# Kernel optimization log

Measured on AMD Instinct MI355X. Metric: run time of the kernel, lower is better.

Reference implementation:

```python
import jax, jax.numpy as jnp
import numpy as np

K_HOPS = 2  # number_layers


def _gcn_norm(edge_index, edge_weight, num_nodes):
    # add self loops with weight 1 (PyG gcn_norm default, fill_value=1)
    row, col = edge_index[0], edge_index[1]
    loop = jnp.arange(num_nodes, dtype=edge_index.dtype)
    row = jnp.concatenate([row, loop])
    col = jnp.concatenate([col, loop])
    w = jnp.concatenate([edge_weight, jnp.ones((num_nodes,), edge_weight.dtype)])
    deg = jax.ops.segment_sum(w, col, num_segments=num_nodes)
    dinv = jnp.where(deg > 0, jax.lax.rsqrt(deg), 0.0)
    norm = dinv[row] * w * dinv[col]
    return row, col, norm


def setup_inputs() -> dict:
    key = jax.random.key(0)
    k1, k2, k3, k4 = jax.random.split(key, 4)
    N, E, F_IN, F_OUT = 100000, 1600000, 256, 40
    x = jax.random.normal(k1, (N, F_IN), dtype=jnp.float32)
    edge_index = jax.random.randint(k2, (2, E), 0, N, dtype=jnp.int64)
    edge_attr = jax.random.uniform(k3, (E,), dtype=jnp.float32)
    W = jax.random.normal(k4, (F_OUT, F_IN), dtype=jnp.float32) * (1.0 / np.sqrt(F_IN))
    b = jnp.zeros((F_OUT,), dtype=jnp.float32)
    return {"x": x, "edge_index": edge_index, "edge_attr": edge_attr, "W": W, "b": b}


def reference(x, edge_index, edge_attr, W, b):
    N = x.shape[0]
    row, col, norm = _gcn_norm(edge_index, edge_attr, N)
    for _ in range(K_HOPS):
        x = jax.ops.segment_sum(norm[:, None] * x[row], col, num_segments=N)
    out = x @ W.T + b           # SGConv final linear
    out = jax.nn.relu(out)      # dropout is a no-op in eval mode
    return jax.nn.log_softmax(out, axis=-1)
```

## Files before the change

kernel.cpp:

```cpp
#include <hip/hip_runtime.h>
#include <hip/hip_bf16.h>
#include <math.h>

#define TF_IN   256
#define TF_OUT  40
#define NCHUNK  (TF_OUT / 4)
#define BCAP    48
#define WQ      32767.0f


__device__ inline float bf2f(unsigned short u) {
    union { unsigned int i; float f; } t; t.i = ((unsigned int)u) << 16; return t.f;
}
__device__ inline unsigned short f2bf(float f) {
    union { float f; unsigned int i; } t; t.f = f;
    unsigned int r = t.i + 0x7FFF + ((t.i >> 16) & 1);
    return (unsigned short)(r >> 16);
}

__global__ void zero_kernel(int* __restrict__ cnt, int N) {
    int i = blockIdx.x * blockDim.x + threadIdx.x;
    if (i < N) cnt[i] = 0;
}

__global__ __launch_bounds__(256) void fused_gemm_scatter_kernel(
        const float* __restrict__ x, const float* __restrict__ W,
        unsigned short* __restrict__ h, int N, int gemmBlocks,
        const int* __restrict__ row, const int* __restrict__ col,
        const float* __restrict__ w, int* __restrict__ cnt,
        unsigned int* __restrict__ bucket, int E) {
    __shared__ float4 xs[128][8];
    __shared__ float4 wsm[40][9];
    int tid = threadIdx.x;

    if ((int)blockIdx.x < gemmBlocks) {
        int ng = tid >> 2;
        int jg = tid & 3;
        int j0 = jg * 10;
        int nodeBase = blockIdx.x * 128;
        int sk = (ng >> 1) & 7;

        float acc[2][10];
#pragma unroll
        for (int i = 0; i < 2; ++i)
#pragma unroll
            for (int j = 0; j < 10; ++j) acc[i][j] = 0.f;

        const float4* x4 = (const float4*)x;
        const float4* W4 = (const float4*)W;

        for (int kt = 0; kt < 8; ++kt) {
            int kb4 = kt * 8;
#pragma unroll
            for (int i = 0; i < 4; ++i) {
                int idx = tid + i * 256;
                int n = idx >> 3, c4 = idx & 7;
                int gn = nodeBase + n;
                float4 v = make_float4(0.f, 0.f, 0.f, 0.f);
                if (gn < N) v = x4[(size_t)gn * (TF_IN / 4) + kb4 + c4];
                xs[n][c4 ^ ((n >> 2) & 7)] = v;
            }
            {
                int idx = tid;
                int j = idx >> 3, c4 = idx & 7;
                wsm[j][c4] = W4[(size_t)j * (TF_IN / 4) + kb4 + c4];
                if (tid < 64) {
                    idx = tid + 256;
                    j = idx >> 3; c4 = idx & 7;
                    wsm[j][c4] = W4[(size_t)j * (TF_IN / 4) + kb4 + c4];
                }
            }
            __syncthreads();
#pragma unroll 2
            for (int c4 = 0; c4 < 8; ++c4) {
                int phys = c4 ^ sk;
                float4 xv0 = xs[ng * 2][phys];
                float4 xv1 = xs[ng * 2 + 1][phys];
#pragma unroll
                for (int jj = 0; jj < 10; ++jj) {
                    float4 wv = wsm[j0 + jj][c4];
                    acc[0][jj] += xv0.x * wv.x + xv0.y * wv.y + xv0.z * wv.z + xv0.w * wv.w;
                    acc[1][jj] += xv1.x * wv.x + xv1.y * wv.y + xv1.z * wv.z + xv1.w * wv.w;
                }
            }
            __syncthreads();
        }

#pragma unroll
        for (int i = 0; i < 2; ++i) {
            int gn = nodeBase + ng * 2 + i;
            if (gn < N) {
                ushort2* hp2 = (ushort2*)(h + (size_t)gn * TF_OUT + j0);
#pragma unroll
                for (int p = 0; p < 5; ++p) {
                    ushort2 o;
                    o.x = f2bf(acc[i][2 * p]);
                    o.y = f2bf(acc[i][2 * p + 1]);
                    hp2[p] = o;
                }
            }
        }
    } else {
        int e = (blockIdx.x - gemmBlocks) * 256 + tid;
        if (e < E) {
            int c = col[e];
            int pos = atomicAdd(&cnt[c], 1);
            if (pos < BCAP) {
                unsigned int wq = (unsigned int)(w[e] * WQ + 0.5f);
                bucket[(size_t)c * BCAP + pos] = ((unsigned int)row[e] << 15) | wq;
            }
        }
    }
}

__global__ void deg_kernel(const unsigned int* __restrict__ bucket, const int* __restrict__ cnt,
                           float* __restrict__ dinv, int N) {
    int n = blockIdx.x * blockDim.x + threadIdx.x;
    if (n >= N) return;
    int m = cnt[n]; if (m > BCAP) m = BCAP;
    const unsigned int* b = bucket + (size_t)n * BCAP;
    float s = 1.0f;
    for (int k = 0; k < m; ++k) s += (float)(b[k] & 0x7FFF) * (1.0f / WQ);
    dinv[n] = rsqrtf(s);
}

__global__ void hop_bf_kernel(const ushort4* __restrict__ hin, ushort4* __restrict__ hout,
                              const int* __restrict__ cnt, const unsigned int* __restrict__ bucket,
                              const float* __restrict__ dinv, int N) {
    int t = blockIdx.x * blockDim.x + threadIdx.x;
    int node  = t / NCHUNK;
    int chunk = t % NCHUNK;
    if (node >= N) return;

    float d = dinv[node];
    ushort4 a = hin[(size_t)node * NCHUNK + chunk];
    float4 acc = make_float4(bf2f(a.x) * d, bf2f(a.y) * d, bf2f(a.z) * d, bf2f(a.w) * d);

    int m = cnt[node]; if (m > BCAP) m = BCAP;
    const unsigned int* b = bucket + (size_t)node * BCAP;
    for (int k = 0; k < m; ++k) {
        unsigned int e = b[k];
        unsigned int r = e >> 15;
        float v = dinv[r] * ((float)(e & 0x7FFF) * (1.0f / WQ));
        ushort4 hv = hin[(size_t)r * NCHUNK + chunk];
        acc.x += v * bf2f(hv.x);
        acc.y += v * bf2f(hv.y);
        acc.z += v * bf2f(hv.z);
        acc.w += v * bf2f(hv.w);
    }
    ushort4 o;
    o.x = f2bf(acc.x * d); o.y = f2bf(acc.y * d);
    o.z = f2bf(acc.z * d); o.w = f2bf(acc.w * d);
    hout[(size_t)node * NCHUNK + chunk] = o;
}

__global__ void hop_f32_kernel(const ushort4* __restrict__ hin, float4* __restrict__ hout,
                               const int* __restrict__ cnt, const unsigned int* __restrict__ bucket,
                               const float* __restrict__ dinv, int N) {
    int t = blockIdx.x * blockDim.x + threadIdx.x;
    int node  = t / NCHUNK;
    int chunk = t % NCHUNK;
    if (node >= N) return;

    float d = dinv[node];
    ushort4 a = hin[(size_t)node * NCHUNK + chunk];
    float4 acc = make_float4(bf2f(a.x) * d, bf2f(a.y) * d, bf2f(a.z) * d, bf2f(a.w) * d);

    int m = cnt[node]; if (m > BCAP) m = BCAP;
    const unsigned int* b = bucket + (size_t)node * BCAP;
    for (int k = 0; k < m; ++k) {
        unsigned int e = b[k];
        unsigned int r = e >> 15;
        float v = dinv[r] * ((float)(e & 0x7FFF) * (1.0f / WQ));
        ushort4 hv = hin[(size_t)r * NCHUNK + chunk];
        acc.x += v * bf2f(hv.x);
        acc.y += v * bf2f(hv.y);
        acc.z += v * bf2f(hv.z);
        acc.w += v * bf2f(hv.w);
    }
    float4 o = make_float4(acc.x * d, acc.y * d, acc.z * d, acc.w * d);
    hout[(size_t)node * NCHUNK + chunk] = o;
}

__global__ void epilogue_kernel(float* __restrict__ out, const float* __restrict__ b, int N) {
    int n = blockIdx.x * blockDim.x + threadIdx.x;
    if (n >= N) return;
    float4* o4 = (float4*)out + (size_t)n * NCHUNK;
    float v[TF_OUT];
#pragma unroll
    for (int i = 0; i < NCHUNK; ++i) {
        float4 t = o4[i];
        v[4 * i] = t.x; v[4 * i + 1] = t.y; v[4 * i + 2] = t.z; v[4 * i + 3] = t.w;
    }
    float m = -1e30f;
#pragma unroll
    for (int j = 0; j < TF_OUT; ++j) {
        float t = v[j] + b[j];
        t = fmaxf(t, 0.f);
        v[j] = t;
        m = fmaxf(m, t);
    }
    float s = 0.f;
#pragma unroll
    for (int j = 0; j < TF_OUT; ++j) s += __expf(v[j] - m);
    float lse = m + __logf(s);
#pragma unroll
    for (int i = 0; i < NCHUNK; ++i) {
        float4 t;
        t.x = v[4 * i]     - lse;
        t.y = v[4 * i + 1] - lse;
        t.z = v[4 * i + 2] - lse;
        t.w = v[4 * i + 3] - lse;
        o4[i] = t;
    }
}

extern "C" void kernel_launch(void* const* d_in, const int* in_sizes, int n_in,
                              void* d_out, int out_size, void* d_ws, size_t ws_size,
                              hipStream_t stream) {
    const float* x  = (const float*)d_in[0];
    const int*   ei = (const int*)d_in[1];
    const float* ew = (const float*)d_in[2];
    const float* W  = (const float*)d_in[3];
    const float* b  = (const float*)d_in[4];

    const int F_out = in_sizes[4];
    const int F_in  = in_sizes[3] / F_out;
    const int N     = in_sizes[0] / F_in;
    const int E     = in_sizes[2];
    const int* row = ei;
    const int* col = ei + E;

    char* ws = (char*)d_ws;
    size_t off = 0;
    auto alloc = [&](size_t bytes) {
        void* p = ws + off;
        off += (bytes + 255) & ~(size_t)255;
        return p;
    };

    int*          cnt    = (int*)          alloc((size_t)N * 4);
    float*        dinv   = (float*)        alloc((size_t)N * 4);
    unsigned int* bucket = (unsigned int*) alloc((size_t)N * BCAP * 4);
    unsigned short* h0   = (unsigned short*)alloc((size_t)N * TF_OUT * 2);
    unsigned short* h1   = (unsigned short*)alloc((size_t)N * TF_OUT * 2);

    const int tb = 256;
    hipLaunchKernelGGL(zero_kernel, dim3((N + tb - 1) / tb), dim3(tb), 0, stream, cnt, N);

    int gemmBlocks    = (N + 127) / 128;
    int scatterBlocks = (E + 255) / 256;
    hipLaunchKernelGGL(fused_gemm_scatter_kernel, dim3(gemmBlocks + scatterBlocks), dim3(256),
                       0, stream, x, W, h0, N, gemmBlocks, row, col, ew, cnt, bucket, E);

    hipLaunchKernelGGL(deg_kernel, dim3((N + tb - 1) / tb), dim3(tb), 0, stream,
                       bucket, cnt, dinv, N);
    int hopThreads = N * NCHUNK;
    hipLaunchKernelGGL(hop_bf_kernel, dim3((hopThreads + tb - 1) / tb), dim3(tb), 0, stream,
                       (const ushort4*)h0, (ushort4*)h1, cnt, bucket, dinv, N);
    hipLaunchKernelGGL(hop_f32_kernel, dim3((hopThreads + tb - 1) / tb), dim3(tb), 0, stream,
                       (const ushort4*)h1, (float4*)d_out, cnt, bucket, dinv, N);
    hipLaunchKernelGGL(epilogue_kernel, dim3((N + tb - 1) / tb), dim3(tb), 0, stream,
                       (float*)d_out, b, N);
}
```

Measured before the change: 352.3 us.

## Fuse second hop with log-softmax epilogue and widen gather to 8-wide chunks

Each thread in the hop kernels now gathers 8 bf16 features (16-byte loads) instead of 4, and the bucket loop is unrolled by 4 with vector index loads to expose more memory-level parallelism. The second hop is fused with bias, ReLU and log-softmax using a shared-memory reduction across the 5 threads per node, which removes the fp32 intermediate write and reread. The edge scatter now handles 4 edges per thread with vectorized loads. The trade-offs are more registers per thread and fewer threads in flight for the gather.

```diff
diff --git a/kernel.cpp b/kernel.cpp
--- a/kernel.cpp
+++ b/kernel.cpp
@@ -4,10 +4,12 @@
 
 #define TF_IN   256
 #define TF_OUT  40
-#define NCHUNK  (TF_OUT / 4)
+#define NCH2    5
 #define BCAP    48
 #define WQ      32767.0f
 
+
+struct us8 { ushort4 a, b; };
 
 __device__ inline float bf2f(unsigned short u) {
     union { unsigned int i; float f; } t; t.i = ((unsigned int)u) << 16; return t.f;
@@ -16,6 +18,41 @@
     union { float f; unsigned int i; } t; t.f = f;
     unsigned int r = t.i + 0x7FFF + ((t.i >> 16) & 1);
     return (unsigned short)(r >> 16);
+}
+
+__device__ inline void acc8(float* acc, float v, const us8& h) {
+    acc[0] += v * bf2f(h.a.x); acc[1] += v * bf2f(h.a.y);
+    acc[2] += v * bf2f(h.a.z); acc[3] += v * bf2f(h.a.w);
+    acc[4] += v * bf2f(h.b.x); acc[5] += v * bf2f(h.b.y);
+    acc[6] += v * bf2f(h.b.z); acc[7] += v * bf2f(h.b.w);
+}
+
+__device__ inline void gather_acc(float* acc, const us8* __restrict__ hin,
+                                  const unsigned int* __restrict__ b, int m,
+                                  int chunk, const float* __restrict__ dinv) {
+    int k = 0;
+    for (; k + 4 <= m; k += 4) {
+        uint4 e4 = *(const uint4*)(b + k);
+        unsigned int r0 = e4.x >> 15, r1 = e4.y >> 15;
+        unsigned int r2 = e4.z >> 15, r3 = e4.w >> 15;
+        us8 h0 = hin[(size_t)r0 * NCH2 + chunk];
+        us8 h1 = hin[(size_t)r1 * NCH2 + chunk];
+        us8 h2 = hin[(size_t)r2 * NCH2 + chunk];
+        us8 h3 = hin[(size_t)r3 * NCH2 + chunk];
+        float v0 = dinv[r0] * ((float)(e4.x & 0x7FFF) * (1.0f / WQ));
+        float v1 = dinv[r1] * ((float)(e4.y & 0x7FFF) * (1.0f / WQ));
+        float v2 = dinv[r2] * ((float)(e4.z & 0x7FFF) * (1.0f / WQ));
+        float v3 = dinv[r3] * ((float)(e4.w & 0x7FFF) * (1.0f / WQ));
+        acc8(acc, v0, h0); acc8(acc, v1, h1);
+        acc8(acc, v2, h2); acc8(acc, v3, h3);
+    }
+    for (; k < m; ++k) {
+        unsigned int e = b[k];
+        unsigned int r = e >> 15;
+        us8 hv = hin[(size_t)r * NCH2 + chunk];
+        float v = dinv[r] * ((float)(e & 0x7FFF) * (1.0f / WQ));
+        acc8(acc, v, hv);
+    }
 }
 
 __global__ void zero_kernel(int* __restrict__ cnt, int N) {
@@ -101,13 +138,31 @@
             }
         }
     } else {
-        int e = (blockIdx.x - gemmBlocks) * 256 + tid;
-        if (e < E) {
-            int c = col[e];
-            int pos = atomicAdd(&cnt[c], 1);
-            if (pos < BCAP) {
-                unsigned int wq = (unsigned int)(w[e] * WQ + 0.5f);
-                bucket[(size_t)c * BCAP + pos] = ((unsigned int)row[e] << 15) | wq;
+        int base = ((int)blockIdx.x - gemmBlocks) * 1024 + tid * 4;
+        if (base + 4 <= E) {
+            int4   c4v = *(const int4*)(col + base);
+            int4   r4v = *(const int4*)(row + base);
+            float4 w4v = *(const float4*)(w + base);
+            int p0 = atomicAdd(&cnt[c4v.x], 1);
+            int p1 = atomicAdd(&cnt[c4v.y], 1);
+            int p2 = atomicAdd(&cnt[c4v.z], 1);
+            int p3 = atomicAdd(&cnt[c4v.w], 1);
+            if (p0 < BCAP) bucket[(size_t)c4v.x * BCAP + p0] =
+                ((unsigned int)r4v.x << 15) | (unsigned int)(w4v.x * WQ + 0.5f);
+            if (p1 < BCAP) bucket[(size_t)c4v.y * BCAP + p1] =
+                ((unsigned int)r4v.y << 15) | (unsigned int)(w4v.y * WQ + 0.5f);
+            if (p2 < BCAP) bucket[(size_t)c4v.z * BCAP + p2] =
+                ((unsigned int)r4v.z << 15) | (unsigned int)(w4v.z * WQ + 0.5f);
+            if (p3 < BCAP) bucket[(size_t)c4v.w * BCAP + p3] =
+                ((unsigned int)r4v.w << 15) | (unsigned int)(w4v.w * WQ + 0.5f);
+        } else {
+            for (int e = base; e < E; ++e) {
+                int c = col[e];
+                int pos = atomicAdd(&cnt[c], 1);
+                if (pos < BCAP) {
+                    unsigned int wq = (unsigned int)(w[e] * WQ + 0.5f);
+                    bucket[(size_t)c * BCAP + pos] = ((unsigned int)row[e] << 15) | wq;
+                }
             }
         }
     }
@@ -124,94 +179,95 @@
     dinv[n] = rsqrtf(s);
 }
 
-__global__ void hop_bf_kernel(const ushort4* __restrict__ hin, ushort4* __restrict__ hout,
-                              const int* __restrict__ cnt, const unsigned int* __restrict__ bucket,
-                              const float* __restrict__ dinv, int N) {
+__global__ __launch_bounds__(256) void hop_bf_kernel(
+        const us8* __restrict__ hin, us8* __restrict__ hout,
+        const int* __restrict__ cnt, const unsigned int* __restrict__ bucket,
+        const float* __restrict__ dinv, int N) {
     int t = blockIdx.x * blockDim.x + threadIdx.x;
-    int node  = t / NCHUNK;
-    int chunk = t % NCHUNK;
+    int node  = t / NCH2;
+    int chunk = t - node * NCH2;
     if (node >= N) return;
 
     float d = dinv[node];
-    ushort4 a = hin[(size_t)node * NCHUNK + chunk];
-    float4 acc = make_float4(bf2f(a.x) * d, bf2f(a.y) * d, bf2f(a.z) * d, bf2f(a.w) * d);
+    us8 a = hin[(size_t)node * NCH2 + chunk];
+    float acc[8];
+    acc[0] = bf2f(a.a.x) * d; acc[1] = bf2f(a.a.y) * d;
+    acc[2] = bf2f(a.a.z) * d; acc[3] = bf2f(a.a.w) * d;
+    acc[4] = bf2f(a.b.x) * d; acc[5] = bf2f(a.b.y) * d;
+    acc[6] = bf2f(a.b.z) * d; acc[7] = bf2f(a.b.w) * d;
 
     int m = cnt[node]; if (m > BCAP) m = BCAP;
-    const unsigned int* b = bucket + (size_t)node * BCAP;
-    for (int k = 0; k < m; ++k) {
-        unsigned int e = b[k];
-        unsigned int r = e >> 15;
-        float v = dinv[r] * ((float)(e & 0x7FFF) * (1.0f / WQ));
-        ushort4 hv = hin[(size_t)r * NCHUNK + chunk];
-        acc.x += v * bf2f(hv.x);
-        acc.y += v * bf2f(hv.y);
-        acc.z += v * bf2f(hv.z);
-        acc.w += v * bf2f(hv.w);
-    }
-    ushort4 o;
-    o.x = f2bf(acc.x * d); o.y = f2bf(acc.y * d);
-    o.z = f2bf(acc.z * d); o.w = f2bf(acc.w * d);
-    hout[(size_t)node * NCHUNK + chunk] = o;
-}
-
-__global__ void hop_f32_kernel(const ushort4* __restrict__ hin, float4* __restrict__ hout,
-                               const int* __restrict__ cnt, const unsigned int* __restrict__ bucket,
-                               const float* __restrict__ dinv, int N) {
-    int t = blockIdx.x * blockDim.x + threadIdx.x;
-    int node  = t / NCHUNK;
-    int chunk = t % NCHUNK;
-    if (node >= N) return;
-
-    float d = dinv[node];
-    ushort4 a = hin[(size_t)node * NCHUNK + chunk];
-    float4 acc = make_float4(bf2f(a.x) * d, bf2f(a.y) * d, bf2f(a.z) * d, bf2f(a.w) * d);
-
-    int m = cnt[node]; if (m > BCAP) m = BCAP;
-    const unsigned int* b = bucket + (size_t)node * BCAP;
-    for (int k = 0; k < m; ++k) {
-        unsigned int e = b[k];
-        unsigned int r = e >> 15;
-        float v = dinv[r] * ((float)(e & 0x7FFF) * (1.0f / WQ));
-        ushort4 hv = hin[(size_t)r * NCHUNK + chunk];
-        acc.x += v * bf2f(hv.x);
-        acc.y += v * bf2f(hv.y);
-        acc.z += v * bf2f(hv.z);
-        acc.w += v * bf2f(hv.w);
-    }
-    float4 o = make_float4(acc.x * d, acc.y * d, acc.z * d, acc.w * d);
-    hout[(size_t)node * NCHUNK + chunk] = o;
-}
-
-__global__ void epilogue_kernel(float* __restrict__ out, const float* __restrict__ b, int N) {
-    int n = blockIdx.x * blockDim.x + threadIdx.x;
-    if (n >= N) return;
-    float4* o4 = (float4*)out + (size_t)n * NCHUNK;
-    float v[TF_OUT];
-#pragma unroll
-    for (int i = 0; i < NCHUNK; ++i) {
-        float4 t = o4[i];
-        v[4 * i] = t.x; v[4 * i + 1] = t.y; v[4 * i + 2] = t.z; v[4 * i + 3] = t.w;
-    }
-    float m = -1e30f;
-#pragma unroll
-    for (int j = 0; j < TF_OUT; ++j) {
-        float t = v[j] + b[j];
-        t = fmaxf(t, 0.f);
-        v[j] = t;
-        m = fmaxf(m, t);
-    }
-    float s = 0.f;
-#pragma unroll
-    for (int j = 0; j < TF_OUT; ++j) s += __expf(v[j] - m);
-    float lse = m + __logf(s);
-#pragma unroll
-    for (int i = 0; i < NCHUNK; ++i) {
-        float4 t;
-        t.x = v[4 * i]     - lse;
-        t.y = v[4 * i + 1] - lse;
-        t.z = v[4 * i + 2] - lse;
-        t.w = v[4 * i + 3] - lse;
-        o4[i] = t;
+    gather_acc(acc, hin, bucket + (size_t)node * BCAP, m, chunk, dinv);
+
+    us8 o;
+    o.a.x = f2bf(acc[0] * d); o.a.y = f2bf(acc[1] * d);
+    o.a.z = f2bf(acc[2] * d); o.a.w = f2bf(acc[3] * d);
+    o.b.x = f2bf(acc[4] * d); o.b.y = f2bf(acc[5] * d);
+    o.b.z = f2bf(acc[6] * d); o.b.w = f2bf(acc[7] * d);
+    hout[(size_t)node * NCH2 + chunk] = o;
+}
+
+__global__ __launch_bounds__(320) void hop2_epi_kernel(
+        const us8* __restrict__ hin, float4* __restrict__ out,
+        const int* __restrict__ cnt, const unsigned int* __restrict__ bucket,
+        const float* __restrict__ dinv, const float* __restrict__ bias, int N) {
+    __shared__ float redm[320];
+    __shared__ float reds[320];
+    int tid = threadIdx.x;
+    int g = tid / NCH2;
+    int chunk = tid - g * NCH2;
+    int node = blockIdx.x * 64 + g;
+    bool valid = node < N;
+
+    float acc[8];
+#pragma unroll
+    for (int j = 0; j < 8; ++j) acc[j] = 0.f;
+    float d = 0.f;
+    if (valid) {
+        d = dinv[node];
+        us8 a = hin[(size_t)node * NCH2 + chunk];
+        acc[0] = bf2f(a.a.x) * d; acc[1] = bf2f(a.a.y) * d;
+        acc[2] = bf2f(a.a.z) * d; acc[3] = bf2f(a.a.w) * d;
+        acc[4] = bf2f(a.b.x) * d; acc[5] = bf2f(a.b.y) * d;
+        acc[6] = bf2f(a.b.z) * d; acc[7] = bf2f(a.b.w) * d;
+        int m = cnt[node]; if (m > BCAP) m = BCAP;
+        gather_acc(acc, hin, bucket + (size_t)node * BCAP, m, chunk, dinv);
+    }
+
+    float v[8];
+    float lm = -1e30f;
+    if (valid) {
+#pragma unroll
+        for (int j = 0; j < 8; ++j) {
+            float t2 = acc[j] * d + bias[chunk * 8 + j];
+            t2 = fmaxf(t2, 0.f);
+            v[j] = t2;
+            lm = fmaxf(lm, t2);
+        }
+    }
+    redm[tid] = lm;
+    __syncthreads();
+    float gm = redm[g * NCH2];
+#pragma unroll
+    for (int i = 1; i < NCH2; ++i) gm = fmaxf(gm, redm[g * NCH2 + i]);
+
+    float ps = 0.f;
+    if (valid) {
+#pragma unroll
+        for (int j = 0; j < 8; ++j) ps += __expf(v[j] - gm);
+    }
+    reds[tid] = ps;
+    __syncthreads();
+    float s = reds[g * NCH2];
+#pragma unroll
+    for (int i = 1; i < NCH2; ++i) s += reds[g * NCH2 + i];
+    float lse = gm + __logf(s);
+
+    if (valid) {
+        float4 o0 = make_float4(v[0] - lse, v[1] - lse, v[2] - lse, v[3] - lse);
+        float4 o1 = make_float4(v[4] - lse, v[5] - lse, v[6] - lse, v[7] - lse);
+        out[(size_t)node * 10 + chunk * 2]     = o0;
+        out[(size_t)node * 10 + chunk * 2 + 1] = o1;
     }
 }
 
@@ -249,17 +305,18 @@
     hipLaunchKernelGGL(zero_kernel, dim3((N + tb - 1) / tb), dim3(tb), 0, stream, cnt, N);
 
     int gemmBlocks    = (N + 127) / 128;
-    int scatterBlocks = (E + 255) / 256;
+    int scatterBlocks = (E + 1023) / 1024;
     hipLaunchKernelGGL(fused_gemm_scatter_kernel, dim3(gemmBlocks + scatterBlocks), dim3(256),
                        0, stream, x, W, h0, N, gemmBlocks, row, col, ew, cnt, bucket, E);
 
     hipLaunchKernelGGL(deg_kernel, dim3((N + tb - 1) / tb), dim3(tb), 0, stream,
                        bucket, cnt, dinv, N);
-    int hopThreads = N * NCHUNK;
-    hipLaunchKernelGGL(hop_bf_kernel, dim3((hopThreads + tb - 1) / tb), dim3(tb), 0, stream,
-                       (const ushort4*)h0, (ushort4*)h1, cnt, bucket, dinv, N);
-    hipLaunchKernelGGL(hop_f32_kernel, dim3((hopThreads + tb - 1) / tb), dim3(tb), 0, stream,
-                       (const ushort4*)h1, (float4*)d_out, cnt, bucket, dinv, N);
-    hipLaunchKernelGGL(epilogue_kernel, dim3((N + tb - 1) / tb), dim3(tb), 0, stream,
-                       (float*)d_out, b, N);
-}
+
+    int hop1Threads = N * NCH2;
+    hipLaunchKernelGGL(hop_bf_kernel, dim3((hop1Threads + tb - 1) / tb), dim3(tb), 0, stream,
+                       (const us8*)h0, (us8*)h1, cnt, bucket, dinv, N);
+
+    int hop2Blocks = (N + 63) / 64;
+    hipLaunchKernelGGL(hop2_epi_kernel, dim3(hop2Blocks), dim3(320), 0, stream,
+                       (const us8*)h1, (float4*)d_out, cnt, bucket, dinv, b, N);
+}
```

After: 331.3 us. -6.0%, faster.
